# Kernel tuning notes

Hardware: AMD Instinct MI355X
Metric: run time of the kernel (lower is better)

Reference implementation:

```python
import jax, jax.numpy as jnp
import numpy as np

STEP_SIZE = 0.01
ITERATION = 1.0
F_FORCING = 8.0
N_STEPS = int(round(ITERATION / STEP_SIZE))  # 100 fixed RK4 steps

BATCH = 8192
INPUT_SIZE = 784
SYSTEM_COUNT = 1024
OUTPUT_SIZE = 10


def setup_inputs() -> dict:
    key = jax.random.key(0)
    k_x, k_w1, k_b1, k_w2, k_b2 = jax.random.split(key, 5)
    x = jax.random.normal(k_x, (BATCH, INPUT_SIZE), dtype=jnp.float32)
    # nn.Linear-style params (out_features, in_features)
    s1 = 1.0 / np.sqrt(INPUT_SIZE)
    W1 = jax.random.uniform(k_w1, (SYSTEM_COUNT, INPUT_SIZE), jnp.float32, -s1, s1)
    b1 = jax.random.uniform(k_b1, (SYSTEM_COUNT,), jnp.float32, -s1, s1)
    s2 = 1.0 / np.sqrt(SYSTEM_COUNT)
    W2 = jax.random.uniform(k_w2, (OUTPUT_SIZE, SYSTEM_COUNT), jnp.float32, -s2, s2)
    b2 = jax.random.uniform(k_b2, (OUTPUT_SIZE,), jnp.float32, -s2, s2)
    return {"x": x, "W1": W1, "b1": b1, "W2": W2, "b2": b2}


def _lorenz96(x):
    # (roll(x,-1) - roll(x,2)) * roll(x,1) - x + F   along feature dim 1
    return (jnp.roll(x, -1, axis=1) - jnp.roll(x, 2, axis=1)) * jnp.roll(x, 1, axis=1) - x + F_FORCING


def _rk4_integrate(x0):
    h = jnp.float32(STEP_SIZE)

    def step(x, _):
        k1 = _lorenz96(x)
        k2 = _lorenz96(x + 0.5 * h * k1)
        k3 = _lorenz96(x + 0.5 * h * k2)
        k4 = _lorenz96(x + h * k3)
        x_next = x + (h / 6.0) * (k1 + 2.0 * k2 + 2.0 * k3 + k4)
        return x_next, None

    xT, _ = jax.lax.scan(step, x0, None, length=N_STEPS)
    return xT


def reference(x, W1, b1, W2, b2):
    h = x @ W1.T + b1                 # [B, systemCount]
    h = _rk4_integrate(h)             # RK4 over [0, iteration], step 0.01
    logits = h @ W2.T + b2            # [B, output_size]
    return jax.nn.log_softmax(logits, axis=1)
```

## Files before the change

### kernel.cpp

```cpp
#include <hip/hip_runtime.h>
#include <hip/hip_bf16.h>
#include <math.h>

#define BATCH 8192
#define INSZ 784
#define SYS 1024
#define OUTSZ 10
#define NSTEP 100
#define HSTEP 0.01f
#define FFORCE 8.0f

typedef short short8 __attribute__((ext_vector_type(8)));
typedef float float4v __attribute__((ext_vector_type(4)));

static __device__ __forceinline__ short f2bf(float x) {
    __hip_bfloat16 b = __float2bfloat16(x);
    return __builtin_bit_cast(short, b);
}
static __device__ __forceinline__ float bf2f(short s) {
    unsigned int u = ((unsigned int)(unsigned short)s) << 16;
    return __builtin_bit_cast(float, u);
}

#define BMg 128
#define BNg 128
#define BKg 32
#define LDK 40

__global__ __launch_bounds__(256, 3) void gemm1_kernel(
    const float* __restrict__ x, const float* __restrict__ W1,
    const float* __restrict__ b1, float* __restrict__ h)
{
    __shared__ short Ah[BMg * LDK], Al[BMg * LDK];
    __shared__ short Bh[BNg * LDK], Bl[BNg * LDK];

    const int t  = threadIdx.x;
    const int bm = blockIdx.y * BMg;
    const int bn = blockIdx.x * BNg;

    const int srow = t >> 1;
    const int kq   = (t & 1) * 16;

    const int wv   = t >> 6;
    const int lane = t & 63;
    const int lm   = lane & 15;
    const int q    = lane >> 4;
    const int rb   = (wv & 1) * 64;
    const int cb   = (wv >> 1) * 64;

    float4v acc[4][4];
    #pragma unroll
    for (int i = 0; i < 4; ++i)
        #pragma unroll
        for (int j = 0; j < 4; ++j) {
            acc[i][j][0] = 0.f; acc[i][j][1] = 0.f;
            acc[i][j][2] = 0.f; acc[i][j][3] = 0.f;
        }

    const float* xa0 = x  + (size_t)(bm + srow) * INSZ + kq;
    const float* wb0 = W1 + (size_t)(bn + srow) * INSZ + kq;

    for (int it = 0; it < 25; ++it) {
        const int k0 = it * BKg;
        {
            const bool valid = (k0 + kq) < INSZ;
            float va[16], vb[16];
            if (valid) {
                #pragma unroll
                for (int p = 0; p < 4; ++p) {
                    float4 xv = ((const float4*)(xa0 + k0))[p];
                    float4 bv = ((const float4*)(wb0 + k0))[p];
                    va[4*p+0] = xv.x; va[4*p+1] = xv.y; va[4*p+2] = xv.z; va[4*p+3] = xv.w;
                    vb[4*p+0] = bv.x; vb[4*p+1] = bv.y; vb[4*p+2] = bv.z; vb[4*p+3] = bv.w;
                }
            } else {
                #pragma unroll
                for (int j = 0; j < 16; ++j) { va[j] = 0.f; vb[j] = 0.f; }
            }
            short8 ahi[2], alo[2], bhi[2], blo[2];
            #pragma unroll
            for (int j = 0; j < 16; ++j) {
                short h1 = f2bf(va[j]);
                short l1 = f2bf(va[j] - bf2f(h1));
                short h2 = f2bf(vb[j]);
                short l2 = f2bf(vb[j] - bf2f(h2));
                ahi[j >> 3][j & 7] = h1;  alo[j >> 3][j & 7] = l1;
                bhi[j >> 3][j & 7] = h2;  blo[j >> 3][j & 7] = l2;
            }
            const int base = srow * LDK + kq;
            *(short8*)&Ah[base] = ahi[0];  *(short8*)&Ah[base + 8] = ahi[1];
            *(short8*)&Al[base] = alo[0];  *(short8*)&Al[base + 8] = alo[1];
            *(short8*)&Bh[base] = bhi[0];  *(short8*)&Bh[base + 8] = bhi[1];
            *(short8*)&Bl[base] = blo[0];  *(short8*)&Bl[base + 8] = blo[1];
        }
        __syncthreads();

        short8 bhf[4], blf[4];
        #pragma unroll
        for (int fj = 0; fj < 4; ++fj) {
            const int off = (cb + fj * 16 + lm) * LDK + q * 8;
            bhf[fj] = *(const short8*)&Bh[off];
            blf[fj] = *(const short8*)&Bl[off];
        }
        #pragma unroll
        for (int fi = 0; fi < 4; ++fi) {
            const int off = (rb + fi * 16 + lm) * LDK + q * 8;
            short8 ah = *(const short8*)&Ah[off];
            short8 al = *(const short8*)&Al[off];
            #pragma unroll
            for (int fj = 0; fj < 4; ++fj) {
                acc[fi][fj] = __builtin_amdgcn_mfma_f32_16x16x32_bf16(ah, bhf[fj], acc[fi][fj], 0, 0, 0);
                acc[fi][fj] = __builtin_amdgcn_mfma_f32_16x16x32_bf16(ah, blf[fj], acc[fi][fj], 0, 0, 0);
                acc[fi][fj] = __builtin_amdgcn_mfma_f32_16x16x32_bf16(al, bhf[fj], acc[fi][fj], 0, 0, 0);
            }
        }
        __syncthreads();
    }

    #pragma unroll
    for (int fj = 0; fj < 4; ++fj) {
        const int col  = bn + cb + fj * 16 + lm;
        const float bias = b1[col];
        #pragma unroll
        for (int fi = 0; fi < 4; ++fi) {
            const int row0 = bm + rb + fi * 16 + q * 4;
            #pragma unroll
            for (int r = 0; r < 4; ++r)
                h[(size_t)(row0 + r) * SYS + col] = acc[fi][fj][r] + bias;
        }
    }
}

__global__ __launch_bounds__(256, 4) void rk4_kernel(
    const float* __restrict__ hbuf, const float* __restrict__ W2,
    const float* __restrict__ b2, float* __restrict__ out)
{
    const int lane = threadIdx.x & 63;
    const int w    = threadIdx.x >> 6;
    const int row  = blockIdx.x * 4 + w;

    const int laneL = (lane + 63) & 63;
    const int laneR = (lane + 1) & 63;

    float X[16];
    {
        const float4* h4 = (const float4*)(hbuf + (size_t)row * SYS) + lane * 4;
        float4 v0 = h4[0], v1 = h4[1], v2 = h4[2], v3 = h4[3];
        X[0]=v0.x; X[1]=v0.y; X[2]=v0.z; X[3]=v0.w;
        X[4]=v1.x; X[5]=v1.y; X[6]=v1.z; X[7]=v1.w;
        X[8]=v2.x; X[9]=v2.y; X[10]=v2.z; X[11]=v2.w;
        X[12]=v3.x; X[13]=v3.y; X[14]=v3.z; X[15]=v3.w;
    }

    float acc[16], T[16];

    auto deriv_ip = [&](float (&y)[16]) {
        float left1  = __shfl(y[15], laneL);
        float left2  = __shfl(y[14], laneL);
        float right1 = __shfl(y[0],  laneR);
        float p2 = left2, p1 = left1, cur = y[0];
        #pragma unroll
        for (int i = 0; i < 16; ++i) {
            float yp1 = (i < 15) ? y[i + 1] : right1;
            float nv  = fmaf(yp1 - p2, p1, FFORCE - cur);
            p2 = p1; p1 = cur;
            if (i < 15) cur = y[i + 1];
            y[i] = nv;
        }
    };

    #pragma unroll 1
    for (int s = 0; s < NSTEP; ++s) {
        {
            float left1  = __shfl(X[15], laneL);
            float left2  = __shfl(X[14], laneL);
            float right1 = __shfl(X[0],  laneR);
            #pragma unroll
            for (int i = 0; i < 16; ++i) {
                float yp1 = (i < 15) ? X[i + 1] : right1;
                float ym1 = (i > 0)  ? X[i - 1] : left1;
                float ym2 = (i > 1)  ? X[i - 2] : ((i == 1) ? left1 : left2);
                acc[i] = fmaf(yp1 - ym2, ym1, FFORCE - X[i]);
            }
        }
        #pragma unroll
        for (int i = 0; i < 16; ++i) T[i] = fmaf(0.5f * HSTEP, acc[i], X[i]);
        deriv_ip(T);
        #pragma unroll
        for (int i = 0; i < 16; ++i) {
            acc[i] = fmaf(2.0f, T[i], acc[i]);
            T[i]   = fmaf(0.5f * HSTEP, T[i], X[i]);
        }
        deriv_ip(T);
        #pragma unroll
        for (int i = 0; i < 16; ++i) {
            acc[i] = fmaf(2.0f, T[i], acc[i]);
            T[i]   = fmaf(HSTEP, T[i], X[i]);
        }
        deriv_ip(T);
        #pragma unroll
        for (int i = 0; i < 16; ++i)
            X[i] = fmaf(HSTEP / 6.0f, acc[i] + T[i], X[i]);
    }

    float l[OUTSZ];
    #pragma unroll
    for (int o = 0; o < OUTSZ; ++o) {
        const float4* w4 = (const float4*)(W2 + (size_t)o * SYS) + lane * 4;
        float4 a = w4[0], b = w4[1], c = w4[2], d = w4[3];
        float s = 0.f;
        s = fmaf(X[0],  a.x, s); s = fmaf(X[1],  a.y, s);
        s = fmaf(X[2],  a.z, s); s = fmaf(X[3],  a.w, s);
        s = fmaf(X[4],  b.x, s); s = fmaf(X[5],  b.y, s);
        s = fmaf(X[6],  b.z, s); s = fmaf(X[7],  b.w, s);
        s = fmaf(X[8],  c.x, s); s = fmaf(X[9],  c.y, s);
        s = fmaf(X[10], c.z, s); s = fmaf(X[11], c.w, s);
        s = fmaf(X[12], d.x, s); s = fmaf(X[13], d.y, s);
        s = fmaf(X[14], d.z, s); s = fmaf(X[15], d.w, s);
        #pragma unroll
        for (int dlt = 1; dlt < 64; dlt <<= 1) s += __shfl_xor(s, dlt);
        l[o] = s + b2[o];
    }

    float m = l[0];
    #pragma unroll
    for (int o = 1; o < OUTSZ; ++o) m = fmaxf(m, l[o]);
    float ssum = 0.f;
    #pragma unroll
    for (int o = 0; o < OUTSZ; ++o) ssum += __expf(l[o] - m);
    const float lse = m + __logf(ssum);

    float v = l[0] - lse;
    #pragma unroll
    for (int o = 1; o < OUTSZ; ++o)
        if (lane == o) v = l[o] - lse;
    if (lane < OUTSZ)
        out[(size_t)row * OUTSZ + lane] = v;
}

extern "C" void kernel_launch(void* const* d_in, const int* in_sizes, int n_in,
                              void* d_out, int out_size, void* d_ws, size_t ws_size,
                              hipStream_t stream)
{
    const float* x  = (const float*)d_in[0];
    const float* W1 = (const float*)d_in[1];
    const float* b1 = (const float*)d_in[2];
    const float* W2 = (const float*)d_in[3];
    const float* b2 = (const float*)d_in[4];
    float* out = (float*)d_out;
    float* h   = (float*)d_ws;

    dim3 g1(SYS / BNg, BATCH / BMg);
    gemm1_kernel<<<g1, 256, 0, stream>>>(x, W1, b1, h);

    rk4_kernel<<<BATCH / 4, 256, 0, stream>>>(h, W2, b2, out);
}
```

Measured before the change: 505.2 us.

## Pack RK4 state into float2 halves to use packed FP32 FMA

Each lane now holds 8 elements from the first half of the row and 8 from the second half, packed as float2 vectors so that the Lorenz-96 updates and RK4 combinations can use packed FP32 FMA instructions. Halo values are exchanged with twice as many scalar shuffles. At the wrap lanes the two components are swapped so the periodic boundary stays correct. The aim is to halve the VALU instruction count of the compute-bound integration loop. In exchange, the extra shuffles and the swap selects add cost, and the benefit depends on the compiler actually emitting v_pk_fma_f32.

```diff
diff --git a/kernel.cpp b/kernel.cpp
--- a/kernel.cpp
+++ b/kernel.cpp
@@ -12,6 +12,7 @@
 
 typedef short short8 __attribute__((ext_vector_type(8)));
 typedef float float4v __attribute__((ext_vector_type(4)));
+typedef float v2f __attribute__((ext_vector_type(2)));
 
 static __device__ __forceinline__ short f2bf(float x) {
     __hip_bfloat16 b = __float2bfloat16(x);
@@ -20,6 +21,19 @@
 static __device__ __forceinline__ float bf2f(short s) {
     unsigned int u = ((unsigned int)(unsigned short)s) << 16;
     return __builtin_bit_cast(float, u);
+}
+
+static __device__ __forceinline__ v2f pkfma(v2f a, v2f b, v2f c) {
+    return __builtin_elementwise_fma(a, b, c);
+}
+static __device__ __forceinline__ v2f mk2(float x, float y) {
+    v2f r; r.x = x; r.y = y; return r;
+}
+static __device__ __forceinline__ v2f swp(v2f v) {
+    return __builtin_shufflevector(v, v, 1, 0);
+}
+static __device__ __forceinline__ v2f sh2(v2f v, int ln) {
+    v2f r; r.x = __shfl(v.x, ln); r.y = __shfl(v.y, ln); return r;
 }
 
 #define BMg 128
@@ -141,82 +155,93 @@
 
     const int laneL = (lane + 63) & 63;
     const int laneR = (lane + 1) & 63;
-
-    float X[16];
+    const bool atL  = (lane == 0);
+    const bool atR  = (lane == 63);
+
+    v2f X[8];
     {
-        const float4* h4 = (const float4*)(hbuf + (size_t)row * SYS) + lane * 4;
-        float4 v0 = h4[0], v1 = h4[1], v2 = h4[2], v3 = h4[3];
-        X[0]=v0.x; X[1]=v0.y; X[2]=v0.z; X[3]=v0.w;
-        X[4]=v1.x; X[5]=v1.y; X[6]=v1.z; X[7]=v1.w;
-        X[8]=v2.x; X[9]=v2.y; X[10]=v2.z; X[11]=v2.w;
-        X[12]=v3.x; X[13]=v3.y; X[14]=v3.z; X[15]=v3.w;
-    }
-
-    float acc[16], T[16];
-
-    auto deriv_ip = [&](float (&y)[16]) {
-        float left1  = __shfl(y[15], laneL);
-        float left2  = __shfl(y[14], laneL);
-        float right1 = __shfl(y[0],  laneR);
-        float p2 = left2, p1 = left1, cur = y[0];
-        #pragma unroll
-        for (int i = 0; i < 16; ++i) {
-            float yp1 = (i < 15) ? y[i + 1] : right1;
-            float nv  = fmaf(yp1 - p2, p1, FFORCE - cur);
+        const float4* b4 = (const float4*)(hbuf + (size_t)row * SYS);
+        float4 a0 = b4[lane * 2], a1 = b4[lane * 2 + 1];
+        float4 c0 = b4[128 + lane * 2], c1 = b4[129 + lane * 2];
+        X[0] = mk2(a0.x, c0.x); X[1] = mk2(a0.y, c0.y);
+        X[2] = mk2(a0.z, c0.z); X[3] = mk2(a0.w, c0.w);
+        X[4] = mk2(a1.x, c1.x); X[5] = mk2(a1.y, c1.y);
+        X[6] = mk2(a1.z, c1.z); X[7] = mk2(a1.w, c1.w);
+    }
+
+    const v2f Fv = mk2(FFORCE, FFORCE);
+    v2f acc[8], T[8];
+
+    auto deriv_ip = [&](v2f (&y)[8]) {
+        v2f r1 = sh2(y[0], laneR);  r1 = atR ? swp(r1) : r1;
+        v2f l1 = sh2(y[7], laneL);  l1 = atL ? swp(l1) : l1;
+        v2f l2 = sh2(y[6], laneL);  l2 = atL ? swp(l2) : l2;
+        v2f p2 = l2, p1 = l1, cur = y[0];
+        #pragma unroll
+        for (int i = 0; i < 8; ++i) {
+            v2f yp1 = (i < 7) ? y[i + 1] : r1;
+            v2f nv  = pkfma(yp1 - p2, p1, Fv - cur);
             p2 = p1; p1 = cur;
-            if (i < 15) cur = y[i + 1];
+            if (i < 7) cur = y[i + 1];
             y[i] = nv;
         }
     };
+
+    const v2f c_half = mk2(0.5f * HSTEP, 0.5f * HSTEP);
+    const v2f c_full = mk2(HSTEP, HSTEP);
+    const v2f c_two  = mk2(2.0f, 2.0f);
+    const v2f c_six  = mk2(HSTEP / 6.0f, HSTEP / 6.0f);
 
     #pragma unroll 1
     for (int s = 0; s < NSTEP; ++s) {
         {
-            float left1  = __shfl(X[15], laneL);
-            float left2  = __shfl(X[14], laneL);
-            float right1 = __shfl(X[0],  laneR);
-            #pragma unroll
-            for (int i = 0; i < 16; ++i) {
-                float yp1 = (i < 15) ? X[i + 1] : right1;
-                float ym1 = (i > 0)  ? X[i - 1] : left1;
-                float ym2 = (i > 1)  ? X[i - 2] : ((i == 1) ? left1 : left2);
-                acc[i] = fmaf(yp1 - ym2, ym1, FFORCE - X[i]);
-            }
-        }
-        #pragma unroll
-        for (int i = 0; i < 16; ++i) T[i] = fmaf(0.5f * HSTEP, acc[i], X[i]);
+            v2f r1 = sh2(X[0], laneR);  r1 = atR ? swp(r1) : r1;
+            v2f l1 = sh2(X[7], laneL);  l1 = atL ? swp(l1) : l1;
+            v2f l2 = sh2(X[6], laneL);  l2 = atL ? swp(l2) : l2;
+            #pragma unroll
+            for (int i = 0; i < 8; ++i) {
+                v2f yp1 = (i < 7) ? X[i + 1] : r1;
+                v2f ym1 = (i > 0) ? X[i - 1] : l1;
+                v2f ym2 = (i > 1) ? X[i - 2] : ((i == 1) ? l1 : l2);
+                acc[i] = pkfma(yp1 - ym2, ym1, Fv - X[i]);
+            }
+        }
+        #pragma unroll
+        for (int i = 0; i < 8; ++i) T[i] = pkfma(c_half, acc[i], X[i]);
         deriv_ip(T);
         #pragma unroll
-        for (int i = 0; i < 16; ++i) {
-            acc[i] = fmaf(2.0f, T[i], acc[i]);
-            T[i]   = fmaf(0.5f * HSTEP, T[i], X[i]);
+        for (int i = 0; i < 8; ++i) {
+            acc[i] = pkfma(c_two, T[i], acc[i]);
+            T[i]   = pkfma(c_half, T[i], X[i]);
         }
         deriv_ip(T);
         #pragma unroll
-        for (int i = 0; i < 16; ++i) {
-            acc[i] = fmaf(2.0f, T[i], acc[i]);
-            T[i]   = fmaf(HSTEP, T[i], X[i]);
+        for (int i = 0; i < 8; ++i) {
+            acc[i] = pkfma(c_two, T[i], acc[i]);
+            T[i]   = pkfma(c_full, T[i], X[i]);
         }
         deriv_ip(T);
         #pragma unroll
-        for (int i = 0; i < 16; ++i)
-            X[i] = fmaf(HSTEP / 6.0f, acc[i] + T[i], X[i]);
+        for (int i = 0; i < 8; ++i)
+            X[i] = pkfma(c_six, acc[i] + T[i], X[i]);
     }
 
     float l[OUTSZ];
     #pragma unroll
     for (int o = 0; o < OUTSZ; ++o) {
-        const float4* w4 = (const float4*)(W2 + (size_t)o * SYS) + lane * 4;
-        float4 a = w4[0], b = w4[1], c = w4[2], d = w4[3];
-        float s = 0.f;
-        s = fmaf(X[0],  a.x, s); s = fmaf(X[1],  a.y, s);
-        s = fmaf(X[2],  a.z, s); s = fmaf(X[3],  a.w, s);
-        s = fmaf(X[4],  b.x, s); s = fmaf(X[5],  b.y, s);
-        s = fmaf(X[6],  b.z, s); s = fmaf(X[7],  b.w, s);
-        s = fmaf(X[8],  c.x, s); s = fmaf(X[9],  c.y, s);
-        s = fmaf(X[10], c.z, s); s = fmaf(X[11], c.w, s);
-        s = fmaf(X[12], d.x, s); s = fmaf(X[13], d.y, s);
-        s = fmaf(X[14], d.z, s); s = fmaf(X[15], d.w, s);
+        const float4* w4 = (const float4*)(W2 + (size_t)o * SYS);
+        float4 wa0 = w4[lane * 2], wa1 = w4[lane * 2 + 1];
+        float4 wc0 = w4[128 + lane * 2], wc1 = w4[129 + lane * 2];
+        v2f s2 = mk2(0.f, 0.f);
+        s2 = pkfma(X[0], mk2(wa0.x, wc0.x), s2);
+        s2 = pkfma(X[1], mk2(wa0.y, wc0.y), s2);
+        s2 = pkfma(X[2], mk2(wa0.z, wc0.z), s2);
+        s2 = pkfma(X[3], mk2(wa0.w, wc0.w), s2);
+        s2 = pkfma(X[4], mk2(wa1.x, wc1.x), s2);
+        s2 = pkfma(X[5], mk2(wa1.y, wc1.y), s2);
+        s2 = pkfma(X[6], mk2(wa1.z, wc1.z), s2);
+        s2 = pkfma(X[7], mk2(wa1.w, wc1.w), s2);
+        float s = s2.x + s2.y;
         #pragma unroll
         for (int dlt = 1; dlt < 64; dlt <<= 1) s += __shfl_xor(s, dlt);
         l[o] = s + b2[o];
```

After: 454.7 us. 10.0% less time.
